# Kernel optimization log

Hardware: AMD Instinct MI355X
Metric: run time of the kernel (lower is better)

Reference implementation:

```python
import jax, jax.numpy as jnp
import numpy as np

S, B, C = 7, 2, 80
L_COORD, L_NOOBJ = 5.0, 0.5
BSZ, N = 8192, 8


def _iou(b1, b2, eps=1e-6):
    ix1 = jnp.maximum(b1[..., 0], b2[..., 0])
    iy1 = jnp.maximum(b1[..., 1], b2[..., 1])
    ix2 = jnp.minimum(b1[..., 2], b2[..., 2])
    iy2 = jnp.minimum(b1[..., 3], b2[..., 3])
    inter = jnp.maximum(ix2 - ix1, 0.0) * jnp.maximum(iy2 - iy1, 0.0)
    a1 = jnp.maximum(b1[..., 2] - b1[..., 0], 0.0) * jnp.maximum(b1[..., 3] - b1[..., 1], 0.0)
    a2 = jnp.maximum(b2[..., 2] - b2[..., 0], 0.0) * jnp.maximum(b2[..., 3] - b2[..., 1], 0.0)
    return inter / (a1 + a2 - inter + eps)


def setup_inputs() -> dict:
    key = jax.random.key(0)
    kp, kb, kl = jax.random.split(key, 3)
    preds = jax.random.normal(kp, (BSZ, S, S, B * 5 + C), dtype=jnp.float32)
    pts = jax.random.uniform(kb, (BSZ, N, 2, 2), dtype=jnp.float32)  # [...,axis(x/y),2pts]
    lo = jnp.min(pts, -1)
    hi = jnp.max(pts, -1)
    hi = jnp.minimum(lo + jnp.maximum(hi - lo, 0.02), 1.0)  # min size so sqrt(w) well-behaved
    gt_boxes = jnp.stack((lo[..., 0], lo[..., 1], hi[..., 0], hi[..., 1]), -1)  # [BSZ,N,4] xyxy
    gt_labels = jax.random.randint(kl, (BSZ, N), 0, C, dtype=jnp.int32)
    return {"preds": preds, "gt_boxes": gt_boxes, "gt_labels": gt_labels}


def reference(preds, gt_boxes, gt_labels):
    Bsz = preds.shape[0]
    pred_boxes = preds[..., : B * 5].reshape(Bsz, S, S, B, 5)
    pred_cls = preds[..., B * 5 :]

    gx1, gy1, gx2, gy2 = (gt_boxes[..., i] for i in range(4))  # each [Bsz,N]
    gcx, gcy = (gx1 + gx2) / 2, (gy1 + gy2) / 2
    gw, gh = gx2 - gx1, gy2 - gy1
    gi = jnp.clip((gcx * S).astype(jnp.int32), 0, S - 1)  # cell col
    gj = jnp.clip((gcy * S).astype(jnp.int32), 0, S - 1)  # cell row

    # gather predicted boxes of the responsible cell for every GT box: [Bsz,N,B,5]
    bidx = jnp.arange(Bsz)[:, None]
    p_cell = pred_boxes[bidx, gj, gi]
    fi = gi[..., None].astype(preds.dtype)
    fj = gj[..., None].astype(preds.dtype)
    pcx = (p_cell[..., 0] + fi) / S
    pcy = (p_cell[..., 1] + fj) / S
    pw = p_cell[..., 2] ** 2
    ph = p_cell[..., 3] ** 2
    p_xyxy = jnp.stack((pcx - pw / 2, pcy - ph / 2, pcx + pw / 2, pcy + ph / 2), -1)
    ious = _iou(p_xyxy, gt_boxes[:, :, None, :])  # [Bsz,N,B]
    best = jnp.argmax(ious, axis=-1)  # [Bsz,N]
    iou_best = jnp.take_along_axis(ious, best[..., None], axis=-1)[..., 0]
    coord_vals = jnp.stack((gcx * S - gi, gcy * S - gj, jnp.sqrt(gw), jnp.sqrt(gh)), -1)

    obj_mask0 = jnp.zeros((Bsz, S, S, B), bool)
    conf_t0 = jnp.zeros((Bsz, S, S, B), preds.dtype)
    coord_t0 = jnp.zeros((Bsz, S, S, B, 4), preds.dtype)
    cls_t0 = jnp.zeros((Bsz, S, S, C), preds.dtype)
    b = jnp.arange(Bsz)

    def step(carry, xk):
        # sequential over GT index k -> later boxes overwrite earlier (torch loop order)
        om, ct, crt, clt = carry
        gik, gjk, bk, iouk, cvk, lk = xk
        om = om.at[b, gjk, gik, bk].set(True)
        ct = ct.at[b, gjk, gik, bk].set(jax.lax.stop_gradient(iouk))
        crt = crt.at[b, gjk, gik, bk].set(cvk)
        clt = clt.at[b, gjk, gik, lk].set(1.0)
        return (om, ct, crt, clt), None

    xs = (gi.T, gj.T, best.T, iou_best.T, jnp.swapaxes(coord_vals, 0, 1), gt_labels.T)
    (obj_mask, conf_t, coord_t, cls_t), _ = jax.lax.scan(
        step, (obj_mask0, conf_t0, coord_t0, cls_t0), xs
    )

    m = obj_mask.astype(preds.dtype)
    coord_loss = L_COORD * jnp.sum(((pred_boxes[..., :4] - coord_t) ** 2) * m[..., None])
    conf_pred = pred_boxes[..., 4]
    obj_loss = jnp.sum(((conf_pred - conf_t) ** 2) * m)
    noobj_loss = L_NOOBJ * jnp.sum(((conf_pred - conf_t) ** 2) * (1.0 - m))
    cell_m = jnp.any(obj_mask, axis=-1).astype(preds.dtype)
    cls_loss = jnp.sum(((pred_cls - cls_t) ** 2) * cell_m[..., None])
    total = coord_loss + obj_loss + noobj_loss + cls_loss
    return total
```

## Files before the change

kernel.cpp:

```cpp
#include <hip/hip_runtime.h>
#include <cstdint>

#define BSZ   8192
#define NGT   8
#define ROW   90
#define CELLS 49
#define WAVES 4
#define BLOCK 256
#define GRID  512

__global__ void zero_out_kernel(float* out) { out[0] = 0.0f; }

__launch_bounds__(BLOCK, 4)
__global__ void yolo_loss_kernel(const float* __restrict__ preds,
                                 const float* __restrict__ gtb,
                                 const int*   __restrict__ gtl,
                                 float* __restrict__ out)
{
    __shared__ int      s_gi[WAVES][NGT], s_gj[WAVES][NGT];
    __shared__ int      s_best[WAVES][NGT], s_label[WAVES][NGT];
    __shared__ float    s_iou[WAVES][NGT];
    __shared__ float    s_cv[WAVES][NGT][4];
    __shared__ float    s_pb[WAVES][NGT][5];
    __shared__ uint32_t s_bits[WAVES][NGT][3];
    __shared__ unsigned char s_fin[WAVES][NGT], s_rep[WAVES][NGT];
    __shared__ float    s_red[WAVES];

    const int tid  = threadIdx.x;
    const int w    = tid >> 6;
    const int lane = tid & 63;
    const int wave_id = blockIdx.x * WAVES + w;
    const int nwaves  = GRID * WAVES;

    float acc = 0.0f;

    const int iters = (BSZ + nwaves - 1) / nwaves;
    for (int it = 0; it < iters; ++it) {
        const int  b      = wave_id + it * nwaves;
        const bool active = (b < BSZ);

        if (active && lane < NGT) {
            const int k = lane;
            const float* gb = gtb + ((size_t)b * NGT + k) * 4;
            float x1 = gb[0], y1 = gb[1], x2 = gb[2], y2 = gb[3];
            float gcx = (x1 + x2) * 0.5f, gcy = (y1 + y2) * 0.5f;
            float gw = x2 - x1, gh = y2 - y1;
            int gi = (int)(gcx * 7.0f); gi = gi < 0 ? 0 : (gi > 6 ? 6 : gi);
            int gj = (int)(gcy * 7.0f); gj = gj < 0 ? 0 : (gj > 6 ? 6 : gj);
            const float* pc = preds + ((size_t)b * CELLS + gj * 7 + gi) * ROW;
            float p[10];
            #pragma unroll
            for (int i = 0; i < 10; ++i) p[i] = pc[i];
            float ious[2];
            #pragma unroll
            for (int bb = 0; bb < 2; ++bb) {
                float pcx = (p[bb*5+0] + (float)gi) / 7.0f;
                float pcy = (p[bb*5+1] + (float)gj) / 7.0f;
                float pw  = p[bb*5+2] * p[bb*5+2];
                float ph  = p[bb*5+3] * p[bb*5+3];
                float bx1 = pcx - pw * 0.5f, by1 = pcy - ph * 0.5f;
                float bx2 = pcx + pw * 0.5f, by2 = pcy + ph * 0.5f;
                float ix1 = fmaxf(bx1, x1), iy1 = fmaxf(by1, y1);
                float ix2 = fminf(bx2, x2), iy2 = fminf(by2, y2);
                float inter = fmaxf(ix2 - ix1, 0.0f) * fmaxf(iy2 - iy1, 0.0f);
                float a1 = fmaxf(bx2 - bx1, 0.0f) * fmaxf(by2 - by1, 0.0f);
                float a2 = fmaxf(x2 - x1, 0.0f) * fmaxf(y2 - y1, 0.0f);
                ious[bb] = inter / (a1 + a2 - inter + 1e-6f);
            }
            int best = (ious[1] > ious[0]) ? 1 : 0;
            s_gi[w][k] = gi; s_gj[w][k] = gj; s_best[w][k] = best;
            s_iou[w][k] = ious[best];
            s_cv[w][k][0] = gcx * 7.0f - (float)gi;
            s_cv[w][k][1] = gcy * 7.0f - (float)gj;
            s_cv[w][k][2] = sqrtf(gw);
            s_cv[w][k][3] = sqrtf(gh);
            #pragma unroll
            for (int f = 0; f < 5; ++f) s_pb[w][k][f] = p[best*5+f];
            s_label[w][k] = gtl[(size_t)b * NGT + k];
        }
        __syncthreads();

        if (active && lane < NGT) {
            const int k = lane;
            int cell = s_gj[w][k]*7 + s_gi[w][k];
            int slot = cell*2 + s_best[w][k];
            unsigned char fin = 1;
            for (int k2 = k+1; k2 < NGT; ++k2) {
                int slot2 = (s_gj[w][k2]*7 + s_gi[w][k2])*2 + s_best[w][k2];
                if (slot2 == slot) fin = 0;
            }
            unsigned char rep = 1;
            for (int k2 = 0; k2 < k; ++k2)
                if (s_gj[w][k2]*7 + s_gi[w][k2] == cell) rep = 0;
            uint32_t b0 = 0, b1 = 0, b2 = 0;
            if (rep) {
                for (int k2 = 0; k2 < NGT; ++k2) {
                    if (s_gj[w][k2]*7 + s_gi[w][k2] == cell) {
                        int l = s_label[w][k2];
                        if (l < 32)      b0 |= 1u << l;
                        else if (l < 64) b1 |= 1u << (l - 32);
                        else             b2 |= 1u << (l - 64);
                    }
                }
            }
            s_fin[w][k] = fin; s_rep[w][k] = rep;
            s_bits[w][k][0] = b0; s_bits[w][k][1] = b1; s_bits[w][k][2] = b2;
        }
        __syncthreads();

        if (active) {
            if (lane < NGT && s_fin[w][lane]) {
                const int k = lane;
                float c = 0.0f;
                #pragma unroll
                for (int f = 0; f < 4; ++f) {
                    float d = s_pb[w][k][f] - s_cv[w][k][f];
                    c += d * d;
                }
                acc += 5.0f * c;
                float p4 = s_pb[w][k][4];
                float d  = p4 - s_iou[w][k];
                acc += d * d - 0.5f * p4 * p4;
            }
            {
                int g = lane >> 3, sub = lane & 7;
                if (s_rep[w][g]) {
                    int cell = s_gj[w][g]*7 + s_gi[w][g];
                    const float* pcl = preds + ((size_t)b * CELLS + cell) * ROW + 10;
                    uint32_t b0 = s_bits[w][g][0], b1 = s_bits[w][g][1], b2 = s_bits[w][g][2];
                    #pragma unroll
                    for (int t = 0; t < 10; ++t) {
                        int c = sub + (t << 3);
                        float p = pcl[c];
                        uint32_t bit = (c < 32) ? (b0 >> c)
                                     : (c < 64) ? (b1 >> (c - 32))
                                                : (b2 >> (c - 64));
                        float tv = (bit & 1u) ? 1.0f : 0.0f;
                        float d = p - tv;
                        acc += d * d;
                    }
                }
            }
            for (int idx = lane; idx < 98; idx += 64) {
                int cell = idx >> 1;
                float p = preds[((size_t)b * CELLS + cell) * ROW + 4 + 5 * (idx & 1)];
                acc += 0.5f * p * p;
            }
        }
        __syncthreads();
    }

    #pragma unroll
    for (int off = 32; off > 0; off >>= 1)
        acc += __shfl_down(acc, off, 64);
    if (lane == 0) s_red[w] = acc;
    __syncthreads();
    if (tid == 0) {
        float t = 0.0f;
        for (int i = 0; i < WAVES; ++i) t += s_red[i];
        atomicAdd(out, t);
    }
}

extern "C" void kernel_launch(void* const* d_in, const int* in_sizes, int n_in,
                              void* d_out, int out_size, void* d_ws, size_t ws_size,
                              hipStream_t stream) {
    const float* preds = (const float*)d_in[0];
    const float* gtb   = (const float*)d_in[1];
    const int*   gtl   = (const int*)d_in[2];
    float* out = (float*)d_out;

    zero_out_kernel<<<1, 1, 0, stream>>>(out);
    yolo_loss_kernel<<<GRID, BLOCK, 0, stream>>>(preds, gtb, gtl, out);
}
```

Before: 206.3 us.

## Replace shared-memory phases with wave shuffles, one wave per image, two-pass reduction

The per-image work now uses one wave per batch item with a grid sized to the whole batch, and the grid-stride loop is gone. The per-GT tables and duplicate/label-bitmask logic move from shared memory with block-wide barriers into registers exchanged via wave shuffles, so there are no __syncthreads inside the work. Per-wave partial sums go to a workspace buffer and a single-block second kernel sums them, which replaces the zero kernel and global atomics. It also vectorizes the GT box and predicted box loads and raises the occupancy hint, at the cost of all 64 lanes redundantly computing the GT logic.

```diff
diff --git a/kernel.cpp b/kernel.cpp
--- a/kernel.cpp
+++ b/kernel.cpp
@@ -5,160 +5,150 @@
 #define NGT   8
 #define ROW   90
 #define CELLS 49
-#define WAVES 4
 #define BLOCK 256
-#define GRID  512
+#define WPB   4
+#define GRID  (BSZ / WPB)
 
-__global__ void zero_out_kernel(float* out) { out[0] = 0.0f; }
+__launch_bounds__(BLOCK, 8)
+__global__ void yolo_main(const float* __restrict__ preds,
+                          const float* __restrict__ gtb,
+                          const int*   __restrict__ gtl,
+                          float* __restrict__ partial)
+{
+    const int tid  = threadIdx.x;
+    const int lane = tid & 63;
+    const int b    = blockIdx.x * WPB + (tid >> 6);
+    const int k    = lane & 7;
 
-__launch_bounds__(BLOCK, 4)
-__global__ void yolo_loss_kernel(const float* __restrict__ preds,
-                                 const float* __restrict__ gtb,
-                                 const int*   __restrict__ gtl,
-                                 float* __restrict__ out)
-{
-    __shared__ int      s_gi[WAVES][NGT], s_gj[WAVES][NGT];
-    __shared__ int      s_best[WAVES][NGT], s_label[WAVES][NGT];
-    __shared__ float    s_iou[WAVES][NGT];
-    __shared__ float    s_cv[WAVES][NGT][4];
-    __shared__ float    s_pb[WAVES][NGT][5];
-    __shared__ uint32_t s_bits[WAVES][NGT][3];
-    __shared__ unsigned char s_fin[WAVES][NGT], s_rep[WAVES][NGT];
-    __shared__ float    s_red[WAVES];
+    const float4 gb = *(const float4*)(gtb + ((size_t)b * NGT + k) * 4);
+    const float x1 = gb.x, y1 = gb.y, x2 = gb.z, y2 = gb.w;
+    const float gcx = (x1 + x2) * 0.5f, gcy = (y1 + y2) * 0.5f;
+    const float gw = x2 - x1, gh = y2 - y1;
+    int gi = (int)(gcx * 7.0f); gi = gi < 0 ? 0 : (gi > 6 ? 6 : gi);
+    int gj = (int)(gcy * 7.0f); gj = gj < 0 ? 0 : (gj > 6 ? 6 : gj);
+    const int cell = gj * 7 + gi;
 
-    const int tid  = threadIdx.x;
-    const int w    = tid >> 6;
-    const int lane = tid & 63;
-    const int wave_id = blockIdx.x * WAVES + w;
-    const int nwaves  = GRID * WAVES;
+    const float* pc = preds + ((size_t)b * CELLS + cell) * ROW;
+    float p[10];
+    #pragma unroll
+    for (int i = 0; i < 5; ++i) {
+        float2 q = *(const float2*)(pc + 2 * i);
+        p[2*i] = q.x; p[2*i+1] = q.y;
+    }
+
+    float ious[2];
+    #pragma unroll
+    for (int bb = 0; bb < 2; ++bb) {
+        float pcx = (p[bb*5+0] + (float)gi) / 7.0f;
+        float pcy = (p[bb*5+1] + (float)gj) / 7.0f;
+        float pw  = p[bb*5+2] * p[bb*5+2];
+        float ph  = p[bb*5+3] * p[bb*5+3];
+        float bx1 = pcx - pw * 0.5f, by1 = pcy - ph * 0.5f;
+        float bx2 = pcx + pw * 0.5f, by2 = pcy + ph * 0.5f;
+        float ix1 = fmaxf(bx1, x1), iy1 = fmaxf(by1, y1);
+        float ix2 = fminf(bx2, x2), iy2 = fminf(by2, y2);
+        float inter = fmaxf(ix2 - ix1, 0.0f) * fmaxf(iy2 - iy1, 0.0f);
+        float a1 = fmaxf(bx2 - bx1, 0.0f) * fmaxf(by2 - by1, 0.0f);
+        float a2 = fmaxf(x2 - x1, 0.0f) * fmaxf(y2 - y1, 0.0f);
+        ious[bb] = inter / (a1 + a2 - inter + 1e-6f);
+    }
+    const int   best = (ious[1] > ious[0]) ? 1 : 0;
+    const float iou  = ious[best];
+    float cv[4] = { gcx * 7.0f - (float)gi, gcy * 7.0f - (float)gj,
+                    sqrtf(gw), sqrtf(gh) };
+    float pb[5];
+    #pragma unroll
+    for (int f = 0; f < 5; ++f) pb[f] = p[best*5 + f];
+    const int label = gtl[(size_t)b * NGT + k];
+
+    const int slot = cell * 2 + best;
+    int cells[8], slots[8], labels[8];
+    #pragma unroll
+    for (int j = 0; j < 8; ++j) {
+        cells[j]  = __shfl(cell,  j, 64);
+        slots[j]  = __shfl(slot,  j, 64);
+        labels[j] = __shfl(label, j, 64);
+    }
+    int fin = 1, rep = 1;
+    uint32_t m0 = 0, m1 = 0, m2 = 0;
+    #pragma unroll
+    for (int j = 0; j < 8; ++j) {
+        if (j > k && slots[j] == slot) fin = 0;
+        if (j < k && cells[j] == cell) rep = 0;
+        if (cells[j] == cell) {
+            int l = labels[j];
+            if (l < 32)      m0 |= 1u << l;
+            else if (l < 64) m1 |= 1u << (l - 32);
+            else             m2 |= 1u << (l - 64);
+        }
+    }
 
     float acc = 0.0f;
 
-    const int iters = (BSZ + nwaves - 1) / nwaves;
-    for (int it = 0; it < iters; ++it) {
-        const int  b      = wave_id + it * nwaves;
-        const bool active = (b < BSZ);
+    if (lane < 8 && fin) {
+        float c = 0.0f;
+        #pragma unroll
+        for (int f = 0; f < 4; ++f) { float d = pb[f] - cv[f]; c += d * d; }
+        acc += 5.0f * c;
+        float d = pb[4] - iou;
+        acc += d * d - 0.5f * pb[4] * pb[4];
+    }
 
-        if (active && lane < NGT) {
-            const int k = lane;
-            const float* gb = gtb + ((size_t)b * NGT + k) * 4;
-            float x1 = gb[0], y1 = gb[1], x2 = gb[2], y2 = gb[3];
-            float gcx = (x1 + x2) * 0.5f, gcy = (y1 + y2) * 0.5f;
-            float gw = x2 - x1, gh = y2 - y1;
-            int gi = (int)(gcx * 7.0f); gi = gi < 0 ? 0 : (gi > 6 ? 6 : gi);
-            int gj = (int)(gcy * 7.0f); gj = gj < 0 ? 0 : (gj > 6 ? 6 : gj);
-            const float* pc = preds + ((size_t)b * CELLS + gj * 7 + gi) * ROW;
-            float p[10];
+    {
+        const int g = lane >> 3, sub = lane & 7;
+        const int      rep_g = __shfl(rep, g, 64);
+        const uint32_t g0 = __shfl(m0, g, 64);
+        const uint32_t g1 = __shfl(m1, g, 64);
+        const uint32_t g2 = __shfl(m2, g, 64);
+        if (rep_g) {
+            const float* pcl = preds + ((size_t)b * CELLS + cells[g]) * ROW + 10;
             #pragma unroll
-            for (int i = 0; i < 10; ++i) p[i] = pc[i];
-            float ious[2];
-            #pragma unroll
-            for (int bb = 0; bb < 2; ++bb) {
-                float pcx = (p[bb*5+0] + (float)gi) / 7.0f;
-                float pcy = (p[bb*5+1] + (float)gj) / 7.0f;
-                float pw  = p[bb*5+2] * p[bb*5+2];
-                float ph  = p[bb*5+3] * p[bb*5+3];
-                float bx1 = pcx - pw * 0.5f, by1 = pcy - ph * 0.5f;
-                float bx2 = pcx + pw * 0.5f, by2 = pcy + ph * 0.5f;
-                float ix1 = fmaxf(bx1, x1), iy1 = fmaxf(by1, y1);
-                float ix2 = fminf(bx2, x2), iy2 = fminf(by2, y2);
-                float inter = fmaxf(ix2 - ix1, 0.0f) * fmaxf(iy2 - iy1, 0.0f);
-                float a1 = fmaxf(bx2 - bx1, 0.0f) * fmaxf(by2 - by1, 0.0f);
-                float a2 = fmaxf(x2 - x1, 0.0f) * fmaxf(y2 - y1, 0.0f);
-                ious[bb] = inter / (a1 + a2 - inter + 1e-6f);
-            }
-            int best = (ious[1] > ious[0]) ? 1 : 0;
-            s_gi[w][k] = gi; s_gj[w][k] = gj; s_best[w][k] = best;
-            s_iou[w][k] = ious[best];
-            s_cv[w][k][0] = gcx * 7.0f - (float)gi;
-            s_cv[w][k][1] = gcy * 7.0f - (float)gj;
-            s_cv[w][k][2] = sqrtf(gw);
-            s_cv[w][k][3] = sqrtf(gh);
-            #pragma unroll
-            for (int f = 0; f < 5; ++f) s_pb[w][k][f] = p[best*5+f];
-            s_label[w][k] = gtl[(size_t)b * NGT + k];
-        }
-        __syncthreads();
-
-        if (active && lane < NGT) {
-            const int k = lane;
-            int cell = s_gj[w][k]*7 + s_gi[w][k];
-            int slot = cell*2 + s_best[w][k];
-            unsigned char fin = 1;
-            for (int k2 = k+1; k2 < NGT; ++k2) {
-                int slot2 = (s_gj[w][k2]*7 + s_gi[w][k2])*2 + s_best[w][k2];
-                if (slot2 == slot) fin = 0;
-            }
-            unsigned char rep = 1;
-            for (int k2 = 0; k2 < k; ++k2)
-                if (s_gj[w][k2]*7 + s_gi[w][k2] == cell) rep = 0;
-            uint32_t b0 = 0, b1 = 0, b2 = 0;
-            if (rep) {
-                for (int k2 = 0; k2 < NGT; ++k2) {
-                    if (s_gj[w][k2]*7 + s_gi[w][k2] == cell) {
-                        int l = s_label[w][k2];
-                        if (l < 32)      b0 |= 1u << l;
-                        else if (l < 64) b1 |= 1u << (l - 32);
-                        else             b2 |= 1u << (l - 64);
-                    }
-                }
-            }
-            s_fin[w][k] = fin; s_rep[w][k] = rep;
-            s_bits[w][k][0] = b0; s_bits[w][k][1] = b1; s_bits[w][k][2] = b2;
-        }
-        __syncthreads();
-
-        if (active) {
-            if (lane < NGT && s_fin[w][lane]) {
-                const int k = lane;
-                float c = 0.0f;
-                #pragma unroll
-                for (int f = 0; f < 4; ++f) {
-                    float d = s_pb[w][k][f] - s_cv[w][k][f];
-                    c += d * d;
-                }
-                acc += 5.0f * c;
-                float p4 = s_pb[w][k][4];
-                float d  = p4 - s_iou[w][k];
-                acc += d * d - 0.5f * p4 * p4;
-            }
-            {
-                int g = lane >> 3, sub = lane & 7;
-                if (s_rep[w][g]) {
-                    int cell = s_gj[w][g]*7 + s_gi[w][g];
-                    const float* pcl = preds + ((size_t)b * CELLS + cell) * ROW + 10;
-                    uint32_t b0 = s_bits[w][g][0], b1 = s_bits[w][g][1], b2 = s_bits[w][g][2];
-                    #pragma unroll
-                    for (int t = 0; t < 10; ++t) {
-                        int c = sub + (t << 3);
-                        float p = pcl[c];
-                        uint32_t bit = (c < 32) ? (b0 >> c)
-                                     : (c < 64) ? (b1 >> (c - 32))
-                                                : (b2 >> (c - 64));
-                        float tv = (bit & 1u) ? 1.0f : 0.0f;
-                        float d = p - tv;
-                        acc += d * d;
-                    }
-                }
-            }
-            for (int idx = lane; idx < 98; idx += 64) {
-                int cell = idx >> 1;
-                float p = preds[((size_t)b * CELLS + cell) * ROW + 4 + 5 * (idx & 1)];
-                acc += 0.5f * p * p;
+            for (int t = 0; t < 10; ++t) {
+                int c = sub + (t << 3);
+                float pv = pcl[c];
+                uint32_t bit = (c < 32) ? (g0 >> c)
+                             : (c < 64) ? (g1 >> (c - 32))
+                                        : (g2 >> (c - 64));
+                float tv = (bit & 1u) ? 1.0f : 0.0f;
+                float d = pv - tv;
+                acc += d * d;
             }
         }
-        __syncthreads();
+    }
+
+    #pragma unroll
+    for (int rr = 0; rr < 2; ++rr) {
+        int idx = lane + 64 * rr;
+        if (idx < 98) {
+            int cc = idx >> 1;
+            float pv = preds[((size_t)b * CELLS + cc) * ROW + 4 + 5 * (idx & 1)];
+            acc += 0.5f * pv * pv;
+        }
     }
 
     #pragma unroll
     for (int off = 32; off > 0; off >>= 1)
         acc += __shfl_down(acc, off, 64);
-    if (lane == 0) s_red[w] = acc;
+    if (lane == 0) partial[b] = acc;
+}
+
+__global__ void yolo_reduce(const float* __restrict__ partial,
+                            float* __restrict__ out)
+{
+    __shared__ float red[BLOCK / 64];
+    const int tid = threadIdx.x, lane = tid & 63;
+    float s = 0.0f;
+    for (int i = tid; i < BSZ; i += BLOCK) s += partial[i];
+    #pragma unroll
+    for (int off = 32; off > 0; off >>= 1)
+        s += __shfl_down(s, off, 64);
+    if (lane == 0) red[tid >> 6] = s;
     __syncthreads();
     if (tid == 0) {
         float t = 0.0f;
-        for (int i = 0; i < WAVES; ++i) t += s_red[i];
-        atomicAdd(out, t);
+        #pragma unroll
+        for (int i = 0; i < BLOCK / 64; ++i) t += red[i];
+        out[0] = t;
     }
 }
 
@@ -168,8 +158,9 @@
     const float* preds = (const float*)d_in[0];
     const float* gtb   = (const float*)d_in[1];
     const int*   gtl   = (const int*)d_in[2];
-    float* out = (float*)d_out;
+    float* partial = (float*)d_ws;
+    float* out     = (float*)d_out;
 
-    zero_out_kernel<<<1, 1, 0, stream>>>(out);
-    yolo_loss_kernel<<<GRID, BLOCK, 0, stream>>>(preds, gtb, gtl, out);
+    yolo_main<<<GRID, BLOCK, 0, stream>>>(preds, gtb, gtl, partial);
+    yolo_reduce<<<1, BLOCK, 0, stream>>>(partial, out);
 }
```

Result: faster. 199.3 us (-3.4%).
